# Kernel tuning notes

Measured on AMD Instinct MI355X. Metric: run time of the kernel, lower is better.

## Reference

```python
import jax, jax.numpy as jnp
import numpy as np

NUM_HEADS = 8
GROUPS = 32
EPS = 1e-5


def group_norm(x, gamma, beta):
    # x: (b, c, L)
    b, c, L = x.shape
    xg = x.reshape(b, GROUPS, c // GROUPS, L)
    mean = xg.mean(axis=(2, 3), keepdims=True)
    var = xg.var(axis=(2, 3), keepdims=True)
    xn = ((xg - mean) / jnp.sqrt(var + EPS)).reshape(b, c, L)
    return xn * gamma[None, :, None] + beta[None, :, None]


def setup_inputs() -> dict:
    key = jax.random.key(0)
    ks = jax.random.split(key, 8)
    b, c, h, w = 8, 512, 32, 32
    inner = c  # inner_channels == -1 -> channels
    x = jax.random.normal(ks[0], (b, c, h, w), dtype=jnp.float32)
    gamma = jnp.ones((c,), dtype=jnp.float32)
    beta = jnp.zeros((c,), dtype=jnp.float32)
    Wq = jax.random.normal(ks[1], (inner, c), dtype=jnp.float32) * 0.02
    bq = jnp.zeros((inner,), dtype=jnp.float32)
    Wkv = jax.random.normal(ks[2], (2 * inner, c), dtype=jnp.float32) * 0.02
    bkv = jnp.zeros((2 * inner,), dtype=jnp.float32)
    Wo = jax.random.normal(ks[3], (c, inner), dtype=jnp.float32) * 0.02
    bo = jnp.zeros((c,), dtype=jnp.float32)
    return {"x": x, "gamma": gamma, "beta": beta, "Wq": Wq, "bq": bq,
            "Wkv": Wkv, "bkv": bkv, "Wo": Wo, "bo": bo}


def reference(x, gamma, beta, Wq, bq, Wkv, bkv, Wo, bo):
    b, c = x.shape[:2]
    spatial = x.shape[2:]
    L = int(np.prod(spatial))
    inner = Wq.shape[0]
    dh = inner // NUM_HEADS
    scale = dh ** -0.5  # NOTE: applied to BOTH q and k, as in the source

    xr = x.reshape(b, c, L)
    hn = group_norm(xr, gamma, beta)          # norm(x); also serves as context

    # 1x1 Conv1d == channel matmul
    q = jnp.einsum('oc,bcl->bol', Wq, hn) + bq[None, :, None]
    kv = jnp.einsum('oc,bcl->bol', Wkv, hn) + bkv[None, :, None]
    k, v = jnp.split(kv, 2, axis=1)

    # (b, heads, dh, L)
    qh = (q * scale).reshape(b, NUM_HEADS, dh, L)
    kh = (k * scale).reshape(b, NUM_HEADS, dh, L)
    vh = v.reshape(b, NUM_HEADS, dh, L)

    dots = jnp.einsum('bhdt,bhds->bhts', qh, kh)
    attn = jax.nn.softmax(dots.astype(jnp.float32), axis=-1).astype(dots.dtype)
    out = jnp.einsum('bhts,bhds->bhdt', attn, vh)  # (b, heads, dh, L)

    out = out.reshape(b, inner, L)
    # output Linear over the channel dim
    out = jnp.einsum('oc,bcl->bol', Wo, out) + bo[None, :, None]
    return (xr + out).reshape(b, c, *spatial)
```

## Files before the change

### kernel.cpp

```cpp
#include <hip/hip_runtime.h>
#include <math.h>

#define B_ 8
#define C_ 512
#define L_ 1024
#define NH_ 8
#define DH_ 64
#define EPS 1e-5f
#define SCALE 0.125f
#define QSCALE (0.125f * 1.44269504088896f)

typedef __bf16 bf16x8 __attribute__((ext_vector_type(8)));
typedef __bf16 bf16x4 __attribute__((ext_vector_type(4)));
typedef float  f32x4  __attribute__((ext_vector_type(4)));

#define MFMA16(a, b, c) __builtin_amdgcn_mfma_f32_16x16x32_bf16((a), (b), (c), 0, 0, 0)

__device__ __forceinline__ void glds16(const __bf16* g, __bf16* l) {
    __builtin_amdgcn_global_load_lds((const __attribute__((address_space(1))) void*)(g),
                                     (__attribute__((address_space(3))) void*)(l),
                                     16, 0, 0);
}

__global__ __launch_bounds__(256)
void prep_kernel(const float* __restrict__ Wq, const float* __restrict__ Wkv,
                 const float* __restrict__ Wo, __bf16* __restrict__ dst,
                 const float* __restrict__ x, float* __restrict__ stats) {
    __shared__ float rs[256], rss[256];
    int bid = blockIdx.x, tid = threadIdx.x;
    if (bid < 1024) {
        int idx = bid * 256 + tid;
        float4 v;
        if (idx < 65536)        v = ((const float4*)Wq)[idx];
        else if (idx < 196608)  v = ((const float4*)Wkv)[idx - 65536];
        else                    v = ((const float4*)Wo)[idx - 196608];
        bf16x4 o;
        o[0] = (__bf16)v.x; o[1] = (__bf16)v.y; o[2] = (__bf16)v.z; o[3] = (__bf16)v.w;
        ((bf16x4*)dst)[idx] = o;
        return;
    }
    int bg = bid - 1024;
    size_t goff = (size_t)bg * 16 * L_;
    const float4* x4 = (const float4*)(x + goff);
    float s = 0.f, ss = 0.f;
    for (int i = tid; i < 4096; i += 256) {
        float4 v = x4[i];
        s  += v.x + v.y + v.z + v.w;
        ss += v.x * v.x + v.y * v.y + v.z * v.z + v.w * v.w;
    }
    rs[tid] = s; rss[tid] = ss;
    __syncthreads();
    for (int off = 128; off > 0; off >>= 1) {
        if (tid < off) { rs[tid] += rs[tid + off]; rss[tid] += rss[tid + off]; }
        __syncthreads();
    }
    if (tid == 0) {
        const float inv_n = 1.f / 16384.f;
        float mean = rs[0] * inv_n;
        float var  = rss[0] * inv_n - mean * mean;
        stats[bg * 2]     = mean;
        stats[bg * 2 + 1] = rsqrtf(var + EPS);
    }
}

__global__ __launch_bounds__(256)
void gn_apply_kernel(const float* __restrict__ x, const float* __restrict__ gamma,
                     const float* __restrict__ beta, const float* __restrict__ stats,
                     __bf16* __restrict__ hnT) {
    __shared__ __bf16 T[32 * 520];
    const int lt = blockIdx.x, b = blockIdx.y;
    const int tid = threadIdx.x;
    const int l0 = lt * 32;
    const int cbase = tid >> 3, fl = tid & 7;
#pragma unroll
    for (int p = 0; p < 16; ++p) {
        int cc = cbase + p * 32;
        float4 v = *(const float4*)&x[((size_t)b * C_ + cc) * L_ + l0 + fl * 4];
        int bg = b * 32 + (cc >> 4);
        float m = stats[bg * 2], rstd = stats[bg * 2 + 1];
        float ga = gamma[cc] * rstd, be = beta[cc];
        T[(fl * 4 + 0) * 520 + cc] = (__bf16)((v.x - m) * ga + be);
        T[(fl * 4 + 1) * 520 + cc] = (__bf16)((v.y - m) * ga + be);
        T[(fl * 4 + 2) * 520 + cc] = (__bf16)((v.z - m) * ga + be);
        T[(fl * 4 + 3) * 520 + cc] = (__bf16)((v.w - m) * ga + be);
    }
    __syncthreads();
    const int lrow = tid >> 6, cu = tid & 63;
#pragma unroll
    for (int pp = 0; pp < 8; ++pp) {
        int l = pp * 4 + lrow;
        bf16x8 r = *(const bf16x8*)&T[l * 520 + cu * 8];
        *(bf16x8*)&hnT[((size_t)b * L_ + l0 + l) * C_ + cu * 8] = r;
    }
}

__device__ __forceinline__
void gemm_mainloop(const __bf16* __restrict__ A, const __bf16* __restrict__ Bp,
                   __bf16* As, __bf16* Bs, f32x4 acc[4][4]) {
    const int tid = threadIdx.x;
    const int lane = tid & 63, w = tid >> 6;
    const int c = lane & 15, q = lane >> 4;
    const int wm = (w >> 1) * 64, wn = (w & 1) * 64;
    const int l8 = lane >> 3, kgsw = (lane & 7) ^ l8;

    for (int k0 = 0; k0 < 512; k0 += 64) {
#pragma unroll
        for (int i = 0; i < 4; ++i) {
            int chunk = w * 4 + i;
            int row = chunk * 8 + l8;
            glds16(A  + (size_t)row * 512 + k0 + kgsw * 8, &As[chunk * 512]);
            glds16(Bp + (size_t)row * 512 + k0 + kgsw * 8, &Bs[chunk * 512]);
        }
        __syncthreads();
#pragma unroll
        for (int ks = 0; ks < 2; ++ks) {
            const int koff = ((ks * 4 + q) ^ (c & 7)) * 8;
            bf16x8 af[4], bfr[4];
#pragma unroll
            for (int m = 0; m < 4; ++m)
                af[m] = *(const bf16x8*)&As[(wm + m * 16 + c) * 64 + koff];
#pragma unroll
            for (int n = 0; n < 4; ++n)
                bfr[n] = *(const bf16x8*)&Bs[(wn + n * 16 + c) * 64 + koff];
#pragma unroll
            for (int m = 0; m < 4; ++m)
#pragma unroll
                for (int n = 0; n < 4; ++n)
                    acc[m][n] = MFMA16(af[m], bfr[n], acc[m][n]);
        }
        __syncthreads();
    }
}

__global__ __launch_bounds__(256)
void qkv_kernel(const __bf16* __restrict__ Wq_bf, const __bf16* __restrict__ Wkv_bf,
                const __bf16* __restrict__ hnT,
                const float* __restrict__ bq, const float* __restrict__ bkv,
                __bf16* __restrict__ qT, __bf16* __restrict__ kT,
                __bf16* __restrict__ vv) {
    __shared__ __bf16 SMEM[128 * 64 * 2];
    __bf16* As = SMEM;
    __bf16* Bs = SMEM + 128 * 64;
    const int b = blockIdx.y;
    const int xx = blockIdx.x;
    const int sec = xx >> 5, t = xx & 31;
    const __bf16* hb = hnT + (size_t)b * L_ * C_;

    const __bf16 *A, *Bp;
    int m0, n0;
    if (sec < 2) {
        m0 = (t & 3) * 128; n0 = (t >> 2) * 128;
        A  = (sec == 0 ? Wq_bf : Wkv_bf) + (size_t)m0 * 512;
        Bp = hb + (size_t)n0 * 512;
    } else {
        m0 = (t >> 2) * 128; n0 = (t & 3) * 128;
        A  = hb + (size_t)m0 * 512;
        Bp = Wkv_bf + (size_t)(512 + n0) * 512;
    }

    f32x4 acc[4][4];
#pragma unroll
    for (int m = 0; m < 4; ++m)
#pragma unroll
        for (int n = 0; n < 4; ++n)
#pragma unroll
            for (int r = 0; r < 4; ++r) acc[m][n][r] = 0.f;

    gemm_mainloop(A, Bp, As, Bs, acc);

    const int tid = threadIdx.x, lane = tid & 63, w = tid >> 6;
    const int c = lane & 15, q = lane >> 4;
    const int wm = (w >> 1) * 64, wn = (w & 1) * 64;

    __bf16* T2 = SMEM;
    const float* bias = (sec == 0) ? bq : bkv;
    const float scl = (sec == 0) ? QSCALE : SCALE;
#pragma unroll
    for (int mt = 0; mt < 4; ++mt)
#pragma unroll
        for (int nt = 0; nt < 4; ++nt) {
            int n_loc = wn + nt * 16 + c;
            int u4 = (wm >> 2) + mt * 4 + q;
            int u4sw = u4 ^ ((n_loc & 7) << 1);
            bf16x4 ov;
            if (sec < 2) {
                int ob = m0 + wm + mt * 16 + q * 4;
#pragma unroll
                for (int r = 0; r < 4; ++r)
                    ov[r] = (__bf16)((acc[mt][nt][r] + bias[ob + r]) * scl);
            } else {
                float bi = bkv[512 + n0 + n_loc];
#pragma unroll
                for (int r = 0; r < 4; ++r)
                    ov[r] = (__bf16)(acc[mt][nt][r] + bi);
            }
            *(bf16x4*)&T2[n_loc * 128 + u4sw * 4] = ov;
        }
    __syncthreads();
#pragma unroll
    for (int p = 0; p < 8; ++p) {
        int rrow = p * 16 + (tid >> 4);
        int u16 = tid & 15;
        int u4p = (u16 * 2) ^ ((rrow & 7) << 1);
        bf16x8 val = *(const bf16x8*)&T2[rrow * 128 + u4p * 4];
        if (sec < 2) {
            int l = n0 + rrow;
            int og = m0 + u16 * 8;
            int hh = og >> 6, d0 = og & 63;
            __bf16* dstp = (sec == 0) ? qT : kT;
            *(bf16x8*)&dstp[((size_t)(b * NH_ + hh) * L_ + l) * DH_ + d0] = val;
        } else {
            int o = n0 + rrow;
            int lg = m0 + u16 * 8;
            *(bf16x8*)&vv[((size_t)b * C_ + o) * L_ + lg] = val;
        }
    }
}

__global__ __launch_bounds__(256)
void attn_kernel(const __bf16* __restrict__ qT, const __bf16* __restrict__ kT,
                 const __bf16* __restrict__ vv, __bf16* __restrict__ aoT) {
    const int tt = blockIdx.x, h = blockIdx.y, b = blockIdx.z;
    const int t0 = tt * 128;
    __shared__ __bf16 Qs[128 * 64];
    __shared__ __bf16 Ks[64 * 64];
    __shared__ __bf16 Vs[64 * 64];
    __shared__ __bf16 Ones[16 * 64];
    __shared__ __bf16 Ps[128 * 72];

    const int tid = threadIdx.x, lane = tid & 63, w = tid >> 6;
    const int c = lane & 15, q = lane >> 4;
    const int l8 = lane >> 3, kg = (lane & 7) ^ l8;

    const __bf16* qbase = qT + ((size_t)(b * NH_ + h) * L_ + t0) * DH_;
    const __bf16* kbase = kT + (size_t)(b * NH_ + h) * L_ * DH_;
    const __bf16* vbase = vv + (size_t)(b * C_ + h * DH_) * L_;

    {
        int row = tid >> 4, u8 = tid & 15;
        int u8sw = (((u8 >> 1) ^ (row & 7)) << 1) | (u8 & 1);
        float fv = (row == 0) ? 1.f : 0.f;
        bf16x4 val;
        val[0] = (__bf16)fv; val[1] = (__bf16)fv; val[2] = (__bf16)fv; val[3] = (__bf16)fv;
        *(bf16x4*)&Ones[row * 64 + u8sw * 4] = val;
    }
#pragma unroll
    for (int i = 0; i < 4; ++i) {
        int chunk = w * 4 + i;
        int row = chunk * 8 + l8;
        glds16(qbase + (size_t)row * DH_ + kg * 8, &Qs[chunk * 512]);
    }

    f32x4 o_acc[2][4], o_l[2];
#pragma unroll
    for (int n2 = 0; n2 < 2; ++n2) {
#pragma unroll
        for (int dt = 0; dt < 4; ++dt)
#pragma unroll
            for (int r = 0; r < 4; ++r) o_acc[n2][dt][r] = 0.f;
#pragma unroll
        for (int r = 0; r < 4; ++r) o_l[n2][r] = 0.f;
    }

    for (int s0 = 0; s0 < L_; s0 += 64) {
#pragma unroll
        for (int i = 0; i < 2; ++i) {
            int chunk = w * 2 + i;
            int row = chunk * 8 + l8;
            glds16(kbase + (size_t)(s0 + row) * DH_ + kg * 8, &Ks[chunk * 512]);
            glds16(vbase + (size_t)row * L_ + s0 + kg * 8, &Vs[chunk * 512]);
        }
        __syncthreads();

        f32x4 sres[4][2];
#pragma unroll
        for (int mt = 0; mt < 4; ++mt)
#pragma unroll
            for (int r = 0; r < 4; ++r) { sres[mt][0][r] = 0.f; sres[mt][1][r] = 0.f; }
#pragma unroll
        for (int ks = 0; ks < 2; ++ks) {
            const int koff = ((ks * 4 + q) ^ (c & 7)) * 8;
            bf16x8 bQ0 = *(const bf16x8*)&Qs[(w * 32 + c) * 64 + koff];
            bf16x8 bQ1 = *(const bf16x8*)&Qs[(w * 32 + 16 + c) * 64 + koff];
#pragma unroll
            for (int mt = 0; mt < 4; ++mt) {
                bf16x8 aK = *(const bf16x8*)&Ks[(mt * 16 + c) * 64 + koff];
                sres[mt][0] = MFMA16(aK, bQ0, sres[mt][0]);
                sres[mt][1] = MFMA16(aK, bQ1, sres[mt][1]);
            }
        }

#pragma unroll
        for (int n2 = 0; n2 < 2; ++n2) {
            int trow = w * 32 + n2 * 16 + c;
#pragma unroll
            for (int mt = 0; mt < 4; ++mt) {
                bf16x4 pv;
#pragma unroll
                for (int r = 0; r < 4; ++r) pv[r] = (__bf16)exp2f(sres[mt][n2][r]);
                *(bf16x4*)&Ps[trow * 72 + (mt * 4 + q) * 4] = pv;
            }
        }

#pragma unroll
        for (int ks = 0; ks < 2; ++ks) {
            const int koff = ((ks * 4 + q) ^ (c & 7)) * 8;
            bf16x8 aV[4];
#pragma unroll
            for (int dt = 0; dt < 4; ++dt)
                aV[dt] = *(const bf16x8*)&Vs[(dt * 16 + c) * 64 + koff];
            bf16x8 aO = *(const bf16x8*)&Ones[c * 64 + koff];
#pragma unroll
            for (int n2 = 0; n2 < 2; ++n2) {
                bf16x8 bp = *(const bf16x8*)&Ps[(w * 32 + n2 * 16 + c) * 72 + ks * 32 + q * 8];
#pragma unroll
                for (int dt = 0; dt < 4; ++dt)
                    o_acc[n2][dt] = MFMA16(aV[dt], bp, o_acc[n2][dt]);
                o_l[n2] = MFMA16(aO, bp, o_l[n2]);
            }
        }
        __syncthreads();
    }

#pragma unroll
    for (int n2 = 0; n2 < 2; ++n2) {
        float lsum = __shfl(o_l[n2][0], c);
        float linv = 1.f / lsum;
        int tg = t0 + w * 32 + n2 * 16 + c;
        __bf16* aobase = aoT + ((size_t)b * L_ + tg) * C_ + h * DH_;
#pragma unroll
        for (int dt = 0; dt < 4; ++dt) {
            bf16x4 ov;
#pragma unroll
            for (int r = 0; r < 4; ++r) ov[r] = (__bf16)(o_acc[n2][dt][r] * linv);
            *(bf16x4*)&aobase[dt * 16 + q * 4] = ov;
        }
    }
}

__global__ __launch_bounds__(256)
void proj_kernel(const __bf16* __restrict__ aoT, const __bf16* __restrict__ Wo_bf,
                 const float* __restrict__ bo, const float* __restrict__ x,
                 float* __restrict__ out) {
    __shared__ __bf16 As[128 * 64], Bs[128 * 64];
    const int b = blockIdx.y, t = blockIdx.x;
    const int m0 = (t >> 2) * 128;
    const int n0 = (t & 3) * 128;
    const __bf16* A  = aoT + (size_t)b * L_ * C_ + (size_t)m0 * 512;
    const __bf16* Bp = Wo_bf + (size_t)n0 * 512;

    f32x4 acc[4][4];
#pragma unroll
    for (int m = 0; m < 4; ++m)
#pragma unroll
        for (int n = 0; n < 4; ++n)
#pragma unroll
            for (int r = 0; r < 4; ++r) acc[m][n][r] = 0.f;

    gemm_mainloop(A, Bp, As, Bs, acc);

    const int tid = threadIdx.x, lane = tid & 63, w = tid >> 6;
    const int c = lane & 15, q = lane >> 4;
    const int wm = (w >> 1) * 64, wn = (w & 1) * 64;

#pragma unroll
    for (int mt = 0; mt < 4; ++mt)
#pragma unroll
        for (int nt = 0; nt < 4; ++nt) {
            int lb = m0 + wm + mt * 16 + q * 4;
            int o  = n0 + wn + nt * 16 + c;
            float bi = bo[o];
            size_t off = ((size_t)b * C_ + o) * L_ + lb;
            float4 xv = *(const float4*)&x[off];
            float4 rv;
            rv.x = acc[mt][nt][0] + bi + xv.x;
            rv.y = acc[mt][nt][1] + bi + xv.y;
            rv.z = acc[mt][nt][2] + bi + xv.z;
            rv.w = acc[mt][nt][3] + bi + xv.w;
            *(float4*)&out[off] = rv;
        }
}

extern "C" void kernel_launch(void* const* d_in, const int* in_sizes, int n_in,
                              void* d_out, int out_size, void* d_ws, size_t ws_size,
                              hipStream_t stream) {
    const float* x     = (const float*)d_in[0];
    const float* gamma = (const float*)d_in[1];
    const float* beta  = (const float*)d_in[2];
    const float* Wq    = (const float*)d_in[3];
    const float* bq    = (const float*)d_in[4];
    const float* Wkv   = (const float*)d_in[5];
    const float* bkv   = (const float*)d_in[6];
    const float* Wo    = (const float*)d_in[7];
    const float* bo    = (const float*)d_in[8];
    float* out = (float*)d_out;

    __bf16* wsb = (__bf16*)d_ws;
    __bf16* Wq_bf  = wsb;
    __bf16* Wkv_bf = wsb + 262144;
    __bf16* Wo_bf  = wsb + 786432;
    __bf16* hnT    = wsb + 1048576;
    __bf16* qT     = wsb + 5242880;
    __bf16* kT     = wsb + 9437184;
    __bf16* vv     = wsb + 13631488;
    __bf16* aoT    = wsb + 17825792;
    float*  stats  = (float*)(wsb + 22020096);

    prep_kernel<<<dim3(1280), 256, 0, stream>>>(Wq, Wkv, Wo, wsb, x, stats);
    gn_apply_kernel<<<dim3(32, B_), 256, 0, stream>>>(x, gamma, beta, stats, hnT);
    qkv_kernel<<<dim3(96, B_), 256, 0, stream>>>(Wq_bf, Wkv_bf, hnT, bq, bkv, qT, kT, vv);
    attn_kernel<<<dim3(8, NH_, B_), 256, 0, stream>>>(qT, kT, vv, aoT);
    proj_kernel<<<dim3(32, B_), 256, 0, stream>>>(aoT, Wo_bf, bo, x, out);
}
```

Measured before the change: 172.4 us.

## Split attention over key range into two halves with combine kernel

The attention kernel now splits the key/value sequence into two halves. Each block writes unnormalized fp32 partial outputs and row sums to workspace, and a new combine kernel adds the halves and normalizes into bf16. This doubles the attention grid from 512 to 1024 blocks to improve occupancy across CUs, at the cost of extra fp32 global traffic and a kernel launch. The QKV block index mapping is also reordered so that blocks sharing an hn tile are adjacent, for better cache reuse. No max subtraction is involved (the kernel already works without a running max), so summing partials is valid.

Result: slower. 180.1 us (+4.4%).

```diff
diff --git a/kernel.cpp b/kernel.cpp
--- a/kernel.cpp
+++ b/kernel.cpp
@@ -143,17 +143,18 @@
     __bf16* Bs = SMEM + 128 * 64;
     const int b = blockIdx.y;
     const int xx = blockIdx.x;
-    const int sec = xx >> 5, t = xx & 31;
+    const int wt = xx % 12, oi = xx / 12;
+    const int sec = wt >> 2;
     const __bf16* hb = hnT + (size_t)b * L_ * C_;
 
     const __bf16 *A, *Bp;
     int m0, n0;
     if (sec < 2) {
-        m0 = (t & 3) * 128; n0 = (t >> 2) * 128;
+        m0 = (wt & 3) * 128; n0 = oi * 128;
         A  = (sec == 0 ? Wq_bf : Wkv_bf) + (size_t)m0 * 512;
         Bp = hb + (size_t)n0 * 512;
     } else {
-        m0 = (t >> 2) * 128; n0 = (t & 3) * 128;
+        m0 = oi * 128; n0 = (wt & 3) * 128;
         A  = hb + (size_t)m0 * 512;
         Bp = Wkv_bf + (size_t)(512 + n0) * 512;
     }
@@ -219,8 +220,10 @@
 
 __global__ __launch_bounds__(256)
 void attn_kernel(const __bf16* __restrict__ qT, const __bf16* __restrict__ kT,
-                 const __bf16* __restrict__ vv, __bf16* __restrict__ aoT) {
-    const int tt = blockIdx.x, h = blockIdx.y, b = blockIdx.z;
+                 const __bf16* __restrict__ vv, float* __restrict__ OP,
+                 float* __restrict__ Lw) {
+    const int tt = blockIdx.x >> 1, sp = blockIdx.x & 1;
+    const int h = blockIdx.y, b = blockIdx.z;
     const int t0 = tt * 128;
     __shared__ __bf16 Qs[128 * 64];
     __shared__ __bf16 Ks[64 * 64];
@@ -262,7 +265,8 @@
         for (int r = 0; r < 4; ++r) o_l[n2][r] = 0.f;
     }
 
-    for (int s0 = 0; s0 < L_; s0 += 64) {
+    const int send = sp * 512 + 512;
+    for (int s0 = sp * 512; s0 < send; s0 += 64) {
 #pragma unroll
         for (int i = 0; i < 2; ++i) {
             int chunk = w * 2 + i;
@@ -322,19 +326,37 @@
         __syncthreads();
     }
 
+    float* OPb = OP + ((((size_t)sp * B_ + b) * NH_ + h) * L_) * DH_;
+    float* Lb  = Lw + (((size_t)sp * B_ + b) * NH_ + h) * L_;
 #pragma unroll
     for (int n2 = 0; n2 < 2; ++n2) {
-        float lsum = __shfl(o_l[n2][0], c);
-        float linv = 1.f / lsum;
         int tg = t0 + w * 32 + n2 * 16 + c;
-        __bf16* aobase = aoT + ((size_t)b * L_ + tg) * C_ + h * DH_;
-#pragma unroll
-        for (int dt = 0; dt < 4; ++dt) {
-            bf16x4 ov;
-#pragma unroll
-            for (int r = 0; r < 4; ++r) ov[r] = (__bf16)(o_acc[n2][dt][r] * linv);
-            *(bf16x4*)&aobase[dt * 16 + q * 4] = ov;
-        }
+#pragma unroll
+        for (int dt = 0; dt < 4; ++dt)
+            *(f32x4*)&OPb[(size_t)tg * DH_ + dt * 16 + q * 4] = o_acc[n2][dt];
+        if (q == 0) Lb[tg] = o_l[n2][0];
+    }
+}
+
+__global__ __launch_bounds__(256)
+void combine_kernel(const float* __restrict__ OP, const float* __restrict__ Lw,
+                    __bf16* __restrict__ aoT) {
+    const int tt = blockIdx.x, h = blockIdx.y, b = blockIdx.z;
+    const int tid = threadIdx.x;
+    const int d4 = (tid & 15) * 4;
+    const size_t hoff = (((size_t)b * NH_ + h) * L_);
+    const size_t spstride_o = (size_t)B_ * NH_ * L_ * DH_;
+    const size_t spstride_l = (size_t)B_ * NH_ * L_;
+#pragma unroll
+    for (int i = 0; i < 4; ++i) {
+        int t = tt * 64 + (tid >> 4) * 4 + i;
+        f32x4 a = *(const f32x4*)&OP[(hoff + t) * DH_ + d4];
+        f32x4 bb = *(const f32x4*)&OP[spstride_o + (hoff + t) * DH_ + d4];
+        float linv = 1.f / (Lw[hoff + t] + Lw[spstride_l + hoff + t]);
+        bf16x4 ov;
+#pragma unroll
+        for (int r = 0; r < 4; ++r) ov[r] = (__bf16)((a[r] + bb[r]) * linv);
+        *(bf16x4*)&aoT[((size_t)b * L_ + t) * C_ + h * DH_ + d4] = ov;
     }
 }
 
@@ -405,10 +427,13 @@
     __bf16* vv     = wsb + 13631488;
     __bf16* aoT    = wsb + 17825792;
     float*  stats  = (float*)(wsb + 22020096);
+    float*  OP     = (float*)(wsb + 22022144);
+    float*  Lw     = (float*)(wsb + 38799360);
 
     prep_kernel<<<dim3(1280), 256, 0, stream>>>(Wq, Wkv, Wo, wsb, x, stats);
     gn_apply_kernel<<<dim3(32, B_), 256, 0, stream>>>(x, gamma, beta, stats, hnT);
     qkv_kernel<<<dim3(96, B_), 256, 0, stream>>>(Wq_bf, Wkv_bf, hnT, bq, bkv, qT, kT, vv);
-    attn_kernel<<<dim3(8, NH_, B_), 256, 0, stream>>>(qT, kT, vv, aoT);
+    attn_kernel<<<dim3(16, NH_, B_), 256, 0, stream>>>(qT, kT, vv, OP, Lw);
+    combine_kernel<<<dim3(16, NH_, B_), 256, 0, stream>>>(OP, Lw, aoT);
     proj_kernel<<<dim3(32, B_), 256, 0, stream>>>(aoT, Wo_bf, bo, x, out);
 }
```

## Load K/V fragments directly from global in attention and reorder QKV block mapping

Applied to the files above, without the earlier changes.

The attention kernel no longer stages Q, K, V and the ones matrix in shared memory. Each wave keeps its Q fragments in registers, reads K and V fragments straight from global memory (relying on cache), and uses a private per-wave P buffer, so the block-wide __syncthreads in the loop go away. Separately, the QKV GEMM grid index is remapped so blocks sharing the same hn tile are adjacent, which should improve L2 reuse. The trade-off is that the four waves each fetch the same K/V data from global/L2 with less coalesced 16-byte loads, and latency is no longer hidden by async LDS loads.

Measured after the change: 221.2 us. 1.28x slower.

```diff
diff --git a/kernel.cpp b/kernel.cpp
--- a/kernel.cpp
+++ b/kernel.cpp
@@ -143,17 +143,18 @@
     __bf16* Bs = SMEM + 128 * 64;
     const int b = blockIdx.y;
     const int xx = blockIdx.x;
-    const int sec = xx >> 5, t = xx & 31;
+    const int wt = xx % 12, oi = xx / 12;
+    const int sec = wt >> 2;
     const __bf16* hb = hnT + (size_t)b * L_ * C_;
 
     const __bf16 *A, *Bp;
     int m0, n0;
     if (sec < 2) {
-        m0 = (t & 3) * 128; n0 = (t >> 2) * 128;
+        m0 = (wt & 3) * 128; n0 = oi * 128;
         A  = (sec == 0 ? Wq_bf : Wkv_bf) + (size_t)m0 * 512;
         Bp = hb + (size_t)n0 * 512;
     } else {
-        m0 = (t >> 2) * 128; n0 = (t & 3) * 128;
+        m0 = oi * 128; n0 = (wt & 3) * 128;
         A  = hb + (size_t)m0 * 512;
         Bp = Wkv_bf + (size_t)(512 + n0) * 512;
     }
@@ -222,34 +223,26 @@
                  const __bf16* __restrict__ vv, __bf16* __restrict__ aoT) {
     const int tt = blockIdx.x, h = blockIdx.y, b = blockIdx.z;
     const int t0 = tt * 128;
-    __shared__ __bf16 Qs[128 * 64];
-    __shared__ __bf16 Ks[64 * 64];
-    __shared__ __bf16 Vs[64 * 64];
-    __shared__ __bf16 Ones[16 * 64];
-    __shared__ __bf16 Ps[128 * 72];
+    __shared__ __bf16 Ps[4 * 32 * 72];
 
     const int tid = threadIdx.x, lane = tid & 63, w = tid >> 6;
     const int c = lane & 15, q = lane >> 4;
-    const int l8 = lane >> 3, kg = (lane & 7) ^ l8;
 
     const __bf16* qbase = qT + ((size_t)(b * NH_ + h) * L_ + t0) * DH_;
     const __bf16* kbase = kT + (size_t)(b * NH_ + h) * L_ * DH_;
     const __bf16* vbase = vv + (size_t)(b * C_ + h * DH_) * L_;
-
-    {
-        int row = tid >> 4, u8 = tid & 15;
-        int u8sw = (((u8 >> 1) ^ (row & 7)) << 1) | (u8 & 1);
-        float fv = (row == 0) ? 1.f : 0.f;
-        bf16x4 val;
-        val[0] = (__bf16)fv; val[1] = (__bf16)fv; val[2] = (__bf16)fv; val[3] = (__bf16)fv;
-        *(bf16x4*)&Ones[row * 64 + u8sw * 4] = val;
-    }
-#pragma unroll
-    for (int i = 0; i < 4; ++i) {
-        int chunk = w * 4 + i;
-        int row = chunk * 8 + l8;
-        glds16(qbase + (size_t)row * DH_ + kg * 8, &Qs[chunk * 512]);
-    }
+    __bf16* Pw = &Ps[w * 32 * 72];
+
+    bf16x8 bQ[2][2];
+#pragma unroll
+    for (int n2 = 0; n2 < 2; ++n2)
+#pragma unroll
+        for (int ks = 0; ks < 2; ++ks)
+            bQ[n2][ks] = *(const bf16x8*)&qbase[(size_t)(w * 32 + n2 * 16 + c) * DH_ + ks * 32 + q * 8];
+
+    bf16x8 aO;
+#pragma unroll
+    for (int j = 0; j < 8; ++j) aO[j] = (c == 0) ? (__bf16)1.0f : (__bf16)0.0f;
 
     f32x4 o_acc[2][4], o_l[2];
 #pragma unroll
@@ -263,15 +256,6 @@
     }
 
     for (int s0 = 0; s0 < L_; s0 += 64) {
-#pragma unroll
-        for (int i = 0; i < 2; ++i) {
-            int chunk = w * 2 + i;
-            int row = chunk * 8 + l8;
-            glds16(kbase + (size_t)(s0 + row) * DH_ + kg * 8, &Ks[chunk * 512]);
-            glds16(vbase + (size_t)row * L_ + s0 + kg * 8, &Vs[chunk * 512]);
-        }
-        __syncthreads();
-
         f32x4 sres[4][2];
 #pragma unroll
         for (int mt = 0; mt < 4; ++mt)
@@ -279,47 +263,39 @@
             for (int r = 0; r < 4; ++r) { sres[mt][0][r] = 0.f; sres[mt][1][r] = 0.f; }
 #pragma unroll
         for (int ks = 0; ks < 2; ++ks) {
-            const int koff = ((ks * 4 + q) ^ (c & 7)) * 8;
-            bf16x8 bQ0 = *(const bf16x8*)&Qs[(w * 32 + c) * 64 + koff];
-            bf16x8 bQ1 = *(const bf16x8*)&Qs[(w * 32 + 16 + c) * 64 + koff];
 #pragma unroll
             for (int mt = 0; mt < 4; ++mt) {
-                bf16x8 aK = *(const bf16x8*)&Ks[(mt * 16 + c) * 64 + koff];
-                sres[mt][0] = MFMA16(aK, bQ0, sres[mt][0]);
-                sres[mt][1] = MFMA16(aK, bQ1, sres[mt][1]);
+                bf16x8 aK = *(const bf16x8*)&kbase[(size_t)(s0 + mt * 16 + c) * DH_ + ks * 32 + q * 8];
+                sres[mt][0] = MFMA16(aK, bQ[0][ks], sres[mt][0]);
+                sres[mt][1] = MFMA16(aK, bQ[1][ks], sres[mt][1]);
             }
         }
 
 #pragma unroll
         for (int n2 = 0; n2 < 2; ++n2) {
-            int trow = w * 32 + n2 * 16 + c;
+            int trow = n2 * 16 + c;
 #pragma unroll
             for (int mt = 0; mt < 4; ++mt) {
                 bf16x4 pv;
 #pragma unroll
                 for (int r = 0; r < 4; ++r) pv[r] = (__bf16)exp2f(sres[mt][n2][r]);
-                *(bf16x4*)&Ps[trow * 72 + (mt * 4 + q) * 4] = pv;
+                *(bf16x4*)&Pw[trow * 72 + (mt * 4 + q) * 4] = pv;
             }
         }
 
 #pragma unroll
-        for (int ks = 0; ks < 2; ++ks) {
-            const int koff = ((ks * 4 + q) ^ (c & 7)) * 8;
-            bf16x8 aV[4];
-#pragma unroll
-            for (int dt = 0; dt < 4; ++dt)
-                aV[dt] = *(const bf16x8*)&Vs[(dt * 16 + c) * 64 + koff];
-            bf16x8 aO = *(const bf16x8*)&Ones[c * 64 + koff];
-#pragma unroll
-            for (int n2 = 0; n2 < 2; ++n2) {
-                bf16x8 bp = *(const bf16x8*)&Ps[(w * 32 + n2 * 16 + c) * 72 + ks * 32 + q * 8];
-#pragma unroll
-                for (int dt = 0; dt < 4; ++dt)
-                    o_acc[n2][dt] = MFMA16(aV[dt], bp, o_acc[n2][dt]);
-                o_l[n2] = MFMA16(aO, bp, o_l[n2]);
+        for (int ksv = 0; ksv < 2; ++ksv) {
+            bf16x8 bp0 = *(const bf16x8*)&Pw[(c) * 72 + ksv * 32 + q * 8];
+            bf16x8 bp1 = *(const bf16x8*)&Pw[(16 + c) * 72 + ksv * 32 + q * 8];
+#pragma unroll
+            for (int dt = 0; dt < 4; ++dt) {
+                bf16x8 aV = *(const bf16x8*)&vbase[(size_t)(dt * 16 + c) * L_ + s0 + ksv * 32 + q * 8];
+                o_acc[0][dt] = MFMA16(aV, bp0, o_acc[0][dt]);
+                o_acc[1][dt] = MFMA16(aV, bp1, o_acc[1][dt]);
             }
-        }
-        __syncthreads();
+            o_l[0] = MFMA16(aO, bp0, o_l[0]);
+            o_l[1] = MFMA16(aO, bp1, o_l[1]);
+        }
     }
 
 #pragma unroll
```
